# Performance work log

Hardware: AMD Instinct MI355X
Metric: run time of the kernel (lower is better)

## Reference

```python
import jax, jax.numpy as jnp
import numpy as np

NEG_INF = -100000000.0  # matches masked_fill value in torch source

def setup_inputs() -> dict:
    key = jax.random.key(0)
    ks = jax.random.split(key, 7)
    d_model, d = 1024, 128
    B, S = 4, 2048
    scale = 1.0 / np.sqrt(d_model)
    x = jax.random.normal(ks[0], (B, S, d_model), dtype=jnp.float32)
    Wq = jax.random.normal(ks[1], (d, d_model), dtype=jnp.float32) * scale
    bq = jax.random.normal(ks[2], (d,), dtype=jnp.float32) * 0.02
    Wk = jax.random.normal(ks[3], (d, d_model), dtype=jnp.float32) * scale
    bk = jax.random.normal(ks[4], (d,), dtype=jnp.float32) * 0.02
    Wv = jax.random.normal(ks[5], (d, d_model), dtype=jnp.float32) * scale
    bv = jax.random.normal(ks[6], (d,), dtype=jnp.float32) * 0.02
    return {"x": x, "Wq": Wq, "bq": bq, "Wk": Wk, "bk": bk, "Wv": Wv, "bv": bv}

def reference(x, Wq, bq, Wk, bk, Wv, bv):
    # Q,K,V: [B,S,d] via torch Linear (x @ W.T + b)
    Q = jnp.einsum('bsm,dm->bsd', x, Wq) + bq
    K = jnp.einsum('bsm,dm->bsd', x, Wk) + bk
    V = jnp.einsum('bsm,dm->bsd', x, Wv) + bv
    d = Wk.shape[0]
    scale = 1.0 / jnp.sqrt(jnp.asarray(d, dtype=Q.dtype))
    scores = jnp.einsum('bqd,bkd->bqk', Q, K) * scale  # [B,S,S]
    # Faithful to source: tril then value-based mask (tril==0 -> -1e8).
    tril = jnp.tril(scores)
    masked = jnp.where(tril == 0, NEG_INF, tril)
    attn = jax.nn.softmax(masked, axis=-1)
    context = jnp.einsum('bqk,bkd->bqd', attn, V)
    return context
```

## Files before the change

### kernel.cpp

```cpp
#include <hip/hip_runtime.h>

typedef __attribute__((ext_vector_type(8))) short bf16x8;
typedef __attribute__((ext_vector_type(4))) float f32x4;

__device__ __forceinline__ unsigned short f2bf(float f) {
    unsigned int u = __float_as_uint(f);
    u += 0x7fffu + ((u >> 16) & 1u);
    return (unsigned short)(u >> 16);
}
__device__ __forceinline__ float bf2f(unsigned short h) {
    return __uint_as_float((unsigned int)h << 16);
}
__device__ __forceinline__ unsigned int cvtpk(float a, float b) {
    unsigned int r;
    asm("v_cvt_pk_bf16_f32 %0, %1, %2" : "=v"(r) : "v"(a), "v"(b));
    return r;
}
__device__ __forceinline__ void async_ld16(void* lds, const void* g) {
    __builtin_amdgcn_global_load_lds(
        (const __attribute__((address_space(1))) unsigned int*)g,
        (__attribute__((address_space(3))) unsigned int*)lds, 16, 0, 0);
}

__global__ __launch_bounds__(256) void conv_w(
    const float* __restrict__ Wq, const float* __restrict__ Wk,
    const float* __restrict__ Wv, unsigned short* __restrict__ Wcat)
{
    size_t o = ((size_t)blockIdx.x * 256 + threadIdx.x) * 8;
    int sel = (int)(o >> 17);
    const float* W = (sel == 0) ? Wq : ((sel == 1) ? Wk : Wv);
    const float* src = W + (o & 131071);
    float4 f0 = ((const float4*)src)[0];
    float4 f1 = ((const float4*)src)[1];
    uint4 u;
    u.x = cvtpk(f0.x, f0.y); u.y = cvtpk(f0.z, f0.w);
    u.z = cvtpk(f1.x, f1.y); u.w = cvtpk(f1.z, f1.w);
    *(uint4*)(Wcat + o) = u;
}

__global__ __launch_bounds__(512, 4) void qkv_gemm(
    const float* __restrict__ x,
    const unsigned short* __restrict__ Wcat,
    const float* __restrict__ bq, const float* __restrict__ bk,
    const float* __restrict__ bv,
    unsigned short* __restrict__ Qf,
    unsigned short* __restrict__ Kf,
    unsigned short* __restrict__ Vf)
{
    __shared__ float Asf[2][32 * 64];
    __shared__ unsigned short Bs[2][128 * 64];

    const int tid  = threadIdx.x;
    const int lane = tid & 63;
    const int w    = tid >> 6;
    const int wm   = w >> 2;
    const int wn   = w & 3;
    const int quad = lane >> 4;
    const int ln   = lane & 15;
    const int lr   = lane >> 3;
    const int csw  = ((lane & 7) ^ lr) * 8;

    const int bid   = blockIdx.x;
    const int nb    = bid >> 8;
    const int mbase = (bid & 255) * 32;
    const unsigned short* Wsel = Wcat + (size_t)nb * 131072;

    const int g = tid;
    const float* asrc = x + (size_t)(mbase + (g >> 4)) * 1024
                          + (size_t)(((g & 15) ^ ((g >> 4) & 15)) * 4);

    f32x4 acc[2];
#pragma unroll
    for (int nt = 0; nt < 2; nt++) acc[nt] = (f32x4){0.f, 0.f, 0.f, 0.f};

    auto stageB = [&](int kb, int p) {
        const int kcol = kb * 64 + csw;
#pragma unroll
        for (int j = 0; j < 2; j++) {
            int chunk = w * 2 + j;
            async_ld16(&Bs[p][chunk * 512 + lane * 8],
                       Wsel + (size_t)(chunk * 8 + lr) * 1024 + kcol);
        }
    };
    auto stageA = [&](int kb, int p) {
        async_ld16(&Asf[p][g * 4], asrc + kb * 64);
    };
    auto readA = [&](int p, int ks) -> bf16x8 {
        const int r = wm * 16 + ln;
        const int J = ks * 4 + quad;
        float4 lo = *(const float4*)&Asf[p][r * 64 + (((2 * J)    ) ^ (r & 15)) * 4];
        float4 hi = *(const float4*)&Asf[p][r * 64 + (((2 * J + 1)) ^ (r & 15)) * 4];
        uint4 u = { cvtpk(lo.x, lo.y), cvtpk(lo.z, lo.w),
                    cvtpk(hi.x, hi.y), cvtpk(hi.z, hi.w) };
        return *reinterpret_cast<const bf16x8*>(&u);
    };

    stageB(0, 0);
    stageA(0, 0);
    __syncthreads();

    for (int kb = 0; kb < 16; kb++) {
        const int p = kb & 1;
        if (kb < 15) {
            stageB(kb + 1, p ^ 1);
            stageA(kb + 1, p ^ 1);
        }
#pragma unroll
        for (int ks = 0; ks < 2; ks++) {
            const int slot = ((ks * 4 + quad) ^ (ln & 7)) * 8;
            bf16x8 a = readA(p, ks);
            bf16x8 b[2];
#pragma unroll
            for (int nt = 0; nt < 2; nt++)
                b[nt] = *(const bf16x8*)&Bs[p][(wn * 32 + nt * 16 + ln) * 64 + slot];
#pragma unroll
            for (int nt = 0; nt < 2; nt++)
                acc[nt] = __builtin_amdgcn_mfma_f32_16x16x32_bf16(a, b[nt], acc[nt], 0, 0, 0);
        }
        __syncthreads();
    }

    const float scale = (nb == 0) ? 0.08838834764831845f : 1.0f;
    const float* bsel = (nb == 0) ? bq : ((nb == 1) ? bk : bv);
    float bias_v[2];
#pragma unroll
    for (int nt = 0; nt < 2; nt++) bias_v[nt] = bsel[wn * 32 + nt * 16 + ln];

    if (nb == 0) {
#pragma unroll
        for (int nt = 0; nt < 2; nt++)
#pragma unroll
            for (int r = 0; r < 4; r++) {
                int m = mbase + wm * 16 + quad * 4 + r;
                int d = wn * 32 + nt * 16 + ln;
                int bb = m >> 11, s = m & 2047;
                int qq = s >> 6, j = s & 63, wv = j >> 4, lnq = j & 15;
                int ksd = d >> 5, rr = d & 31, qd = rr >> 3, e = rr & 7;
                size_t idx = (((size_t)((bb * 32 + qq) * 4 + wv) * 4 + ksd) * 64
                              + qd * 16 + lnq) * 8 + e;
                Qf[idx] = f2bf((acc[nt][r] + bias_v[nt]) * scale);
            }
    } else if (nb == 1) {
#pragma unroll
        for (int nt = 0; nt < 2; nt++)
#pragma unroll
            for (int r = 0; r < 4; r++) {
                int m = mbase + wm * 16 + quad * 4 + r;
                int d = wn * 32 + nt * 16 + ln;
                int bb = m >> 11, s = m & 2047;
                int kt = s >> 6, j = s & 63, ct = j >> 4, lnk = j & 15;
                int ksd = d >> 5, rr = d & 31, qd = rr >> 3, e = rr & 7;
                size_t idx = (((size_t)(bb * 128 + kt * 4 + ct) * 4 + ksd) * 64
                              + qd * 16 + lnk) * 8 + e;
                Kf[idx] = f2bf(acc[nt][r] + bias_v[nt]);
            }
    } else {
#pragma unroll
        for (int nt = 0; nt < 2; nt++) {
            int dd = wn * 32 + nt * 16 + ln;
            int m0 = mbase + wm * 16 + quad * 4;
            int bb = m0 >> 11, s0 = m0 & 2047;
            int kt = s0 >> 6, j0 = s0 & 63;
            int kstep = j0 >> 5, rr0 = j0 & 31, qdv = rr0 >> 3, e0 = rr0 & 7;
            int dt = dd >> 4, lnv = dd & 15;
            size_t base = ((((size_t)(bb * 32 + kt) * 2 + kstep) * 8 + dt) * 64
                           + qdv * 16 + lnv) * 8 + e0;
            ushort4 u = { f2bf(acc[nt][0] + bias_v[nt]),
                          f2bf(acc[nt][1] + bias_v[nt]),
                          f2bf(acc[nt][2] + bias_v[nt]),
                          f2bf(acc[nt][3] + bias_v[nt]) };
            *(ushort4*)&Vf[base] = u;
        }
    }
}

__global__ __launch_bounds__(64, 2) void flash_attn(
    const unsigned short* __restrict__ Qf,
    const unsigned short* __restrict__ Kf,
    const unsigned short* __restrict__ Vf,
    unsigned short* __restrict__ Opart,
    float* __restrict__ lsum_g,
    float* __restrict__ out)
{
    __shared__ unsigned short Pl[16][72];

    const int w = blockIdx.x & 3;
    int j = blockIdx.x >> 2;
    const int b = j / 144;
    int t = j % 144;
    int q = 0, c = 0;
#pragma unroll 1
    for (int qq = 0; qq < 32; qq++) {
        int ncq = (qq >> 2) + 1;
        if (t < ncq) { q = qq; c = t; break; }
        t -= ncq;
    }
    const int m4 = q >> 2, r4 = q & 3;
    const int nc = m4 + 1;
    const int pbase = b * 144 + q + 2 * m4 * (m4 - 1) + r4 * m4;
    const int pidx  = pbase + c;
    const int k0 = c * 4;
    const int kend = (c * 4 + 4 < q + 1) ? (c * 4 + 4) : (q + 1);

    const int lane = threadIdx.x & 63, quad = lane >> 4, ln = lane & 15;
    const float M0 = 16.0f;

    bf16x8 qa[4];
    const unsigned short* qbt =
        Qf + (size_t)((b * 32 + q) * 4 + w) * 2048 + lane * 8;
#pragma unroll
    for (int ks = 0; ks < 4; ks++)
        qa[ks] = *(const bf16x8*)(qbt + (size_t)ks * 512);

    float l_i[4];
    f32x4 Ofr[8];
#pragma unroll
    for (int r = 0; r < 4; r++) l_i[r] = 0.f;
#pragma unroll
    for (int dt = 0; dt < 8; dt++) Ofr[dt] = (f32x4){0.f, 0.f, 0.f, 0.f};

    for (int kt = k0; kt < kend; kt++) {
        const unsigned short* kbt = Kf + (size_t)(b * 128 + kt * 4) * 2048 + lane * 8;
        const unsigned short* vbt = Vf + (size_t)(b * 32 + kt) * 8192 + lane * 8;
        bf16x8 kf[4][4], vf[2][8];
#pragma unroll
        for (int ct = 0; ct < 4; ct++)
#pragma unroll
            for (int ks = 0; ks < 4; ks++)
                kf[ct][ks] = *(const bf16x8*)(kbt + (size_t)(ct * 4 + ks) * 512);
#pragma unroll
        for (int kstep = 0; kstep < 2; kstep++)
#pragma unroll
            for (int dt = 0; dt < 8; dt++)
                vf[kstep][dt] = *(const bf16x8*)(vbt + (size_t)(kstep * 8 + dt) * 512);

        f32x4 sfr[4];
#pragma unroll
        for (int ct = 0; ct < 4; ct++) {
            f32x4 s = (f32x4){0.f, 0.f, 0.f, 0.f};
#pragma unroll
            for (int ks = 0; ks < 4; ks++)
                s = __builtin_amdgcn_mfma_f32_16x16x32_bf16(qa[ks], kf[ct][ks], s, 0, 0, 0);
            sfr[ct] = s;
        }

        if (kt == q) {
#pragma unroll
            for (int ct = 0; ct < 4; ct++)
#pragma unroll
                for (int r = 0; r < 4; r++)
                    if (ct * 16 + ln > w * 16 + quad * 4 + r)
                        sfr[ct][r] = -__builtin_inff();
        }

#pragma unroll
        for (int ct = 0; ct < 4; ct++)
#pragma unroll
            for (int r = 0; r < 4; r++) {
                float pv = __expf(sfr[ct][r] - M0);
                l_i[r] += pv;
                Pl[quad * 4 + r][ct * 16 + ln] = f2bf(pv);
            }

#pragma unroll
        for (int kstep = 0; kstep < 2; kstep++) {
            bf16x8 pa = *(const bf16x8*)&Pl[ln][kstep * 32 + quad * 8];
#pragma unroll
            for (int dt = 0; dt < 8; dt++)
                Ofr[dt] = __builtin_amdgcn_mfma_f32_16x16x32_bf16(pa, vf[kstep][dt], Ofr[dt], 0, 0, 0);
        }
    }

#pragma unroll
    for (int off = 1; off < 16; off <<= 1)
#pragma unroll
        for (int r = 0; r < 4; r++) l_i[r] += __shfl_xor(l_i[r], off, 64);

    if (nc == 1) {
        float inv_[4];
#pragma unroll
        for (int r = 0; r < 4; r++) inv_[r] = 1.0f / l_i[r];
#pragma unroll
        for (int dt = 0; dt < 8; dt++)
#pragma unroll
            for (int r = 0; r < 4; r++) {
                int row = w * 16 + quad * 4 + r;
                out[((size_t)(b * 2048 + q * 64 + row)) * 128 + dt * 16 + ln] =
                    Ofr[dt][r] * inv_[r];
            }
        return;
    }

#pragma unroll
    for (int dt = 0; dt < 8; dt++) {
        ushort4 u = { f2bf(Ofr[dt][0]), f2bf(Ofr[dt][1]),
                      f2bf(Ofr[dt][2]), f2bf(Ofr[dt][3]) };
        *(ushort4*)&Opart[(((size_t)pidx * 8 + dt) * 4 + w) * 256 + lane * 4] = u;
    }
    if (ln == 0) {
#pragma unroll
        for (int r = 0; r < 4; r++)
            lsum_g[(size_t)pidx * 64 + w * 16 + quad * 4 + r] = l_i[r];
    }
}

__global__ __launch_bounds__(256) void combine(
    const unsigned short* __restrict__ Opart,
    const float* __restrict__ lsum_g,
    float* __restrict__ out)
{
    const int j = blockIdx.x;
    const int b = j / 28;
    const int q = (j % 28) + 4;
    const int m4 = q >> 2, r4 = q & 3;
    const int nc = m4 + 1;
    const int pbase = b * 144 + q + 2 * m4 * (m4 - 1) + r4 * m4;

    const int tid  = threadIdx.x;
    const int lane = tid & 63, w = tid >> 6, quad = lane >> 4, ln = lane & 15;

    float lt[4] = {0.f, 0.f, 0.f, 0.f};
    f32x4 Ofr[8];
#pragma unroll
    for (int dt = 0; dt < 8; dt++) Ofr[dt] = (f32x4){0.f, 0.f, 0.f, 0.f};

#pragma unroll 1
    for (int c2 = 0; c2 < nc; c2++) {
        const size_t pb2 = (size_t)(pbase + c2);
#pragma unroll
        for (int r = 0; r < 4; r++)
            lt[r] += lsum_g[pb2 * 64 + w * 16 + quad * 4 + r];
#pragma unroll
        for (int dt = 0; dt < 8; dt++) {
            ushort4 u = *(const ushort4*)&Opart[((pb2 * 8 + dt) * 4 + w) * 256 + lane * 4];
            Ofr[dt][0] += bf2f(u.x);
            Ofr[dt][1] += bf2f(u.y);
            Ofr[dt][2] += bf2f(u.z);
            Ofr[dt][3] += bf2f(u.w);
        }
    }
    float inv_[4];
#pragma unroll
    for (int r = 0; r < 4; r++) inv_[r] = 1.0f / lt[r];
#pragma unroll
    for (int dt = 0; dt < 8; dt++)
#pragma unroll
        for (int r = 0; r < 4; r++) {
            int row = w * 16 + quad * 4 + r;
            out[((size_t)(b * 2048 + q * 64 + row)) * 128 + dt * 16 + ln] =
                Ofr[dt][r] * inv_[r];
        }
}

extern "C" void kernel_launch(void* const* d_in, const int* in_sizes, int n_in,
                              void* d_out, int out_size, void* d_ws, size_t ws_size,
                              hipStream_t stream) {
    const float* x  = (const float*)d_in[0];
    const float* Wq = (const float*)d_in[1];
    const float* bq = (const float*)d_in[2];
    const float* Wk = (const float*)d_in[3];
    const float* bk = (const float*)d_in[4];
    const float* Wv = (const float*)d_in[5];
    const float* bv = (const float*)d_in[6];
    float* out = (float*)d_out;

    char* wsb = (char*)d_ws;
    unsigned short* Opart = (unsigned short*)wsb;
    float*          lsum  = (float*)(wsb + 9437184);
    unsigned short* Wcat  = (unsigned short*)(wsb + 10485760);
    unsigned short* Qf    = (unsigned short*)(wsb + 11272192);
    unsigned short* Kf    = Qf + (size_t)8192 * 128;
    unsigned short* Vf    = Qf + (size_t)2 * 8192 * 128;

    conv_w<<<192, 256, 0, stream>>>(Wq, Wk, Wv, Wcat);
    qkv_gemm<<<768, 512, 0, stream>>>(x, Wcat, bq, bk, bv, Qf, Kf, Vf);
    flash_attn<<<2304, 64, 0, stream>>>(Qf, Kf, Vf, Opart, lsum, out);
    combine<<<112, 256, 0, stream>>>(Opart, lsum, out);
}
```

Baseline: 117.2 us.

## Share K/V tiles across four waves via double-buffered async LDS staging

Merges the four single-wave blocks that handled one query tile into a single 256-thread block, so each K/V tile is loaded once from global memory into LDS and shared by all four waves. The loads use async global-to-LDS copies into a double buffer, prefetching the next tile while the current one is computed, with a block barrier per iteration. This removes redundant global/L2 traffic and register pressure from holding K/V fragments. In exchange it adds about 64KB of LDS per block, which limits occupancy, plus LDS read traffic and barrier stalls.

```diff
diff --git a/kernel.cpp b/kernel.cpp
--- a/kernel.cpp
+++ b/kernel.cpp
@@ -174,7 +174,7 @@
     }
 }
 
-__global__ __launch_bounds__(64, 2) void flash_attn(
+__global__ __launch_bounds__(256, 2) void flash_attn(
     const unsigned short* __restrict__ Qf,
     const unsigned short* __restrict__ Kf,
     const unsigned short* __restrict__ Vf,
@@ -182,10 +182,10 @@
     float* __restrict__ lsum_g,
     float* __restrict__ out)
 {
-    __shared__ unsigned short Pl[16][72];
-
-    const int w = blockIdx.x & 3;
-    int j = blockIdx.x >> 2;
+    __shared__ unsigned short KVs[2][16384];
+    __shared__ unsigned short Pl[64][72];
+
+    int j = blockIdx.x;
     const int b = j / 144;
     int t = j % 144;
     int q = 0, c = 0;
@@ -202,8 +202,20 @@
     const int k0 = c * 4;
     const int kend = (c * 4 + 4 < q + 1) ? (c * 4 + 4) : (q + 1);
 
-    const int lane = threadIdx.x & 63, quad = lane >> 4, ln = lane & 15;
+    const int tid  = threadIdx.x;
+    const int lane = tid & 63, w = tid >> 6, quad = lane >> 4, ln = lane & 15;
     const float M0 = 16.0f;
+
+    auto stageKV = [&](int kt, int p) {
+        const unsigned short* kb = Kf + (size_t)(b * 128 + kt * 4) * 2048;
+        const unsigned short* vb = Vf + (size_t)(b * 32 + kt) * 8192;
+#pragma unroll
+        for (int g = 0; g < 4; g++) {
+            int o = (g * 256 + tid) * 8;
+            async_ld16(&KVs[p][o], kb + o);
+            async_ld16(&KVs[p][8192 + o], vb + o);
+        }
+    };
 
     bf16x8 qa[4];
     const unsigned short* qbt =
@@ -219,28 +231,22 @@
 #pragma unroll
     for (int dt = 0; dt < 8; dt++) Ofr[dt] = (f32x4){0.f, 0.f, 0.f, 0.f};
 
+    stageKV(k0, 0);
+    __syncthreads();
+
+    int p = 0;
     for (int kt = k0; kt < kend; kt++) {
-        const unsigned short* kbt = Kf + (size_t)(b * 128 + kt * 4) * 2048 + lane * 8;
-        const unsigned short* vbt = Vf + (size_t)(b * 32 + kt) * 8192 + lane * 8;
-        bf16x8 kf[4][4], vf[2][8];
-#pragma unroll
-        for (int ct = 0; ct < 4; ct++)
-#pragma unroll
-            for (int ks = 0; ks < 4; ks++)
-                kf[ct][ks] = *(const bf16x8*)(kbt + (size_t)(ct * 4 + ks) * 512);
-#pragma unroll
-        for (int kstep = 0; kstep < 2; kstep++)
-#pragma unroll
-            for (int dt = 0; dt < 8; dt++)
-                vf[kstep][dt] = *(const bf16x8*)(vbt + (size_t)(kstep * 8 + dt) * 512);
+        if (kt + 1 < kend) stageKV(kt + 1, p ^ 1);
 
         f32x4 sfr[4];
 #pragma unroll
         for (int ct = 0; ct < 4; ct++) {
             f32x4 s = (f32x4){0.f, 0.f, 0.f, 0.f};
 #pragma unroll
-            for (int ks = 0; ks < 4; ks++)
-                s = __builtin_amdgcn_mfma_f32_16x16x32_bf16(qa[ks], kf[ct][ks], s, 0, 0, 0);
+            for (int ks = 0; ks < 4; ks++) {
+                bf16x8 kf = *(const bf16x8*)&KVs[p][(ct * 4 + ks) * 512 + lane * 8];
+                s = __builtin_amdgcn_mfma_f32_16x16x32_bf16(qa[ks], kf, s, 0, 0, 0);
+            }
             sfr[ct] = s;
         }
 
@@ -259,16 +265,21 @@
             for (int r = 0; r < 4; r++) {
                 float pv = __expf(sfr[ct][r] - M0);
                 l_i[r] += pv;
-                Pl[quad * 4 + r][ct * 16 + ln] = f2bf(pv);
+                Pl[w * 16 + quad * 4 + r][ct * 16 + ln] = f2bf(pv);
             }
 
 #pragma unroll
         for (int kstep = 0; kstep < 2; kstep++) {
-            bf16x8 pa = *(const bf16x8*)&Pl[ln][kstep * 32 + quad * 8];
-#pragma unroll
-            for (int dt = 0; dt < 8; dt++)
-                Ofr[dt] = __builtin_amdgcn_mfma_f32_16x16x32_bf16(pa, vf[kstep][dt], Ofr[dt], 0, 0, 0);
-        }
+            bf16x8 pa = *(const bf16x8*)&Pl[w * 16 + ln][kstep * 32 + quad * 8];
+#pragma unroll
+            for (int dt = 0; dt < 8; dt++) {
+                bf16x8 vf = *(const bf16x8*)&KVs[p][8192 + (kstep * 8 + dt) * 512 + lane * 8];
+                Ofr[dt] = __builtin_amdgcn_mfma_f32_16x16x32_bf16(pa, vf, Ofr[dt], 0, 0, 0);
+            }
+        }
+
+        __syncthreads();
+        p ^= 1;
     }
 
 #pragma unroll
@@ -374,6 +385,6 @@
 
     conv_w<<<192, 256, 0, stream>>>(Wq, Wk, Wv, Wcat);
     qkv_gemm<<<768, 512, 0, stream>>>(x, Wcat, bq, bk, bv, Qf, Kf, Vf);
-    flash_attn<<<2304, 64, 0, stream>>>(Qf, Kf, Vf, Opart, lsum, out);
+    flash_attn<<<576, 256, 0, stream>>>(Qf, Kf, Vf, Opart, lsum, out);
     combine<<<112, 256, 0, stream>>>(Opart, lsum, out);
 }
```

Measured after the change: 119.8 us. 1.02x slower.
